# Kernel optimization log

Measured on AMD Instinct MI355X. Metric: run time of the kernel, lower is better.

The kernel has to match this reference:

```python
import jax, jax.numpy as jnp
import numpy as np

NUM_SEQS = 128
TOTAL_TOKENS = 65536
HIDDEN = 768
FF = 3072
EPS = 1e-12  # torch F.normalize default eps


def _make_prompt_lens(rng: np.random.Generator) -> np.ndarray:
    # Ragged lengths in [64, 960], adjusted so they sum exactly to TOTAL_TOKENS.
    lens = rng.integers(64, 960, size=NUM_SEQS).astype(np.int64)
    lens = np.maximum(1, (lens * (TOTAL_TOKENS / lens.sum())).astype(np.int64))
    lens[-1] += TOTAL_TOKENS - lens.sum()
    assert lens.sum() == TOTAL_TOKENS and (lens > 0).all()
    return lens


def setup_inputs() -> dict:
    key = jax.random.key(0)
    k1, k2, k3 = jax.random.split(key, 3)
    hidden_states = jax.random.normal(k1, (TOTAL_TOKENS, HIDDEN), dtype=jnp.float32)
    prompt_lens = jnp.asarray(_make_prompt_lens(np.random.default_rng(0)))
    W1 = jax.random.normal(k2, (FF, HIDDEN), dtype=jnp.float32) * (HIDDEN ** -0.5)
    W2 = jax.random.normal(k3, (HIDDEN, FF), dtype=jnp.float32) * (FF ** -0.5)
    return {"hidden_states": hidden_states, "prompt_lens": prompt_lens, "W1": W1, "W2": W2}


def reference(hidden_states, prompt_lens, W1, W2):
    # hidden_states: [T, H]; prompt_lens: [S] summing to T.
    T = hidden_states.shape[0]
    S = prompt_lens.shape[0]
    # segment id of each token: index of first cumsum strictly greater than position
    seg_ids = jnp.searchsorted(jnp.cumsum(prompt_lens), jnp.arange(T), side="right")
    sums = jax.ops.segment_sum(hidden_states, seg_ids, num_segments=S)  # [S, H]
    pooled = sums / prompt_lens[:, None].astype(hidden_states.dtype)     # mean pool
    h = jnp.einsum("sh,fh->sf", pooled, W1)   # dense1: 768 -> 3072 (no bias)
    h = jnp.einsum("sf,hf->sh", h, W2)        # dense2: 3072 -> 768 (no bias)
    norm = jnp.linalg.norm(h, ord=2, axis=-1, keepdims=True)
    return h / jnp.maximum(norm, EPS)         # L2 normalize, [S, H]
```

## Files before the change

### kernel.cpp

```cpp
#include <hip/hip_runtime.h>

#define TOK   65536
#define HID   768
#define NSEQ  128
#define FFD   3072
#define PCH   32
#define NPCH  (TOK / PCH)
#define KS1   8
#define KCH1  96
#define KS2   32
#define KCH2  96

__device__ __forceinline__ void add4(float4& a, const float4 b) {
  a.x += b.x; a.y += b.y; a.z += b.z; a.w += b.w;
}

__device__ __forceinline__ void scan_lens(const int* __restrict__ lens, int* sc, int tid) {
  if (tid < NSEQ) sc[tid] = lens[tid];
  __syncthreads();
  for (int off = 1; off < NSEQ; off <<= 1) {
    int v = 0;
    if (tid < NSEQ && tid >= off) v = sc[tid - off];
    __syncthreads();
    if (tid < NSEQ) sc[tid] += v;
    __syncthreads();
  }
}

__global__ __launch_bounds__(192, 6) void pool_part(
    const float* __restrict__ x, const int* __restrict__ lens,
    float* __restrict__ plo, float* __restrict__ phi) {
  __shared__ int sc[NSEQ];
  const int tid = threadIdx.x;
  scan_lens(lens, sc, tid);
  const int t0 = blockIdx.x * PCH;
  int lo = 0, hi = NSEQ - 1;
  while (lo < hi) { int mid = (lo + hi) >> 1; if (sc[mid] <= t0) lo = mid + 1; else hi = mid; }
  const int segend = sc[lo];
  const float4* p = (const float4*)x + (size_t)t0 * (HID / 4) + tid;
  float4* dlo = (float4*)plo + (size_t)blockIdx.x * (HID / 4) + tid;

  if (segend >= t0 + PCH) {
    float4 a0 = make_float4(0.f,0.f,0.f,0.f), a1 = a0, a2 = a0, a3 = a0;
    #pragma unroll
    for (int i = 0; i < PCH; i += 4) {
      add4(a0, p[(size_t)(i+0) * (HID/4)]);
      add4(a1, p[(size_t)(i+1) * (HID/4)]);
      add4(a2, p[(size_t)(i+2) * (HID/4)]);
      add4(a3, p[(size_t)(i+3) * (HID/4)]);
    }
    add4(a0, a1); add4(a2, a3); add4(a0, a2);
    *dlo = a0;
  } else {
    const int n0 = segend - t0;
    float4 a0 = make_float4(0.f,0.f,0.f,0.f), a1 = a0;
    for (int i = 0;  i < n0;  ++i) add4(a0, p[(size_t)i * (HID/4)]);
    for (int i = n0; i < PCH; ++i) add4(a1, p[(size_t)i * (HID/4)]);
    *dlo = a0;
    *((float4*)phi + (size_t)blockIdx.x * (HID/4) + tid) = a1;
  }
}

__global__ __launch_bounds__(192) void pool_reduce(
    const int* __restrict__ lens, const float* __restrict__ plo,
    const float* __restrict__ phi, float* __restrict__ pooled) {
  __shared__ int sc[NSEQ];
  const int tid = threadIdx.x;
  scan_lens(lens, sc, tid);
  const int s = blockIdx.x;
  const int st = s ? sc[s - 1] : 0;
  const int en = sc[s];
  const int c0 = st >> 5, c1 = (en - 1) >> 5;
  const float4* lo4 = (const float4*)plo;
  const float4* hi4 = (const float4*)phi;
  float4 acc = make_float4(0.f,0.f,0.f,0.f);
  for (int c = c0; c <= c1; ++c) {
    const float4* src = (c == c0 && (st & (PCH - 1))) ? hi4 : lo4;
    add4(acc, src[(size_t)c * (HID / 4) + tid]);
  }
  const float inv = 1.0f / (float)(en - st);
  float4 r;
  r.x = acc.x * inv; r.y = acc.y * inv; r.z = acc.z * inv; r.w = acc.w * inv;
  ((float4*)pooled)[(size_t)s * (HID / 4) + tid] = r;
}

__global__ __launch_bounds__(256) void gemm_nt(
    const float* __restrict__ A, const float* __restrict__ B,
    float* __restrict__ Cp, int N, int Kt, int kch) {
  __shared__ float As[16][132];
  __shared__ float Bs[16][36];

  const int tid = threadIdx.x;
  const int f0 = blockIdx.x * 32;
  const int k0 = blockIdx.y * kch;
  float* C = Cp + (size_t)blockIdx.y * NSEQ * N;
  const int fx = (tid & 7) * 4;
  const int sy = (tid >> 3) * 4;
  const int sA = tid >> 2;
  const int kA = (tid & 3) * 4;
  const int fB = tid >> 2;

  const float* pA0 = A + (size_t)sA * Kt + k0 + kA;
  const float* pA1 = pA0 + (size_t)64 * Kt;
  const float* pB  = B + (size_t)(f0 + fB) * Kt + k0 + kA;

  float4 va0 = *(const float4*)pA0;
  float4 va1 = *(const float4*)pA1;
  float4 vb = make_float4(0.f,0.f,0.f,0.f);
  if (tid < 128) vb = *(const float4*)pB;

  float acc[4][4];
  #pragma unroll
  for (int i = 0; i < 4; ++i)
    #pragma unroll
    for (int j = 0; j < 4; ++j) acc[i][j] = 0.f;

  const int nch = kch >> 4;
  for (int c = 0; c < nch; ++c) {
    As[kA + 0][sA]      = va0.x; As[kA + 1][sA]      = va0.y;
    As[kA + 2][sA]      = va0.z; As[kA + 3][sA]      = va0.w;
    As[kA + 0][sA + 64] = va1.x; As[kA + 1][sA + 64] = va1.y;
    As[kA + 2][sA + 64] = va1.z; As[kA + 3][sA + 64] = va1.w;
    if (tid < 128) {
      Bs[kA + 0][fB] = vb.x; Bs[kA + 1][fB] = vb.y;
      Bs[kA + 2][fB] = vb.z; Bs[kA + 3][fB] = vb.w;
    }
    __syncthreads();
    if (c + 1 < nch) {
      va0 = *(const float4*)(pA0 + (c + 1) * 16);
      va1 = *(const float4*)(pA1 + (c + 1) * 16);
      if (tid < 128) vb = *(const float4*)(pB + (c + 1) * 16);
    }
    #pragma unroll
    for (int kk = 0; kk < 16; ++kk) {
      const float4 aa = *(const float4*)&As[kk][sy];
      const float4 bb = *(const float4*)&Bs[kk][fx];
      acc[0][0] += aa.x*bb.x; acc[0][1] += aa.x*bb.y; acc[0][2] += aa.x*bb.z; acc[0][3] += aa.x*bb.w;
      acc[1][0] += aa.y*bb.x; acc[1][1] += aa.y*bb.y; acc[1][2] += aa.y*bb.z; acc[1][3] += aa.y*bb.w;
      acc[2][0] += aa.z*bb.x; acc[2][1] += aa.z*bb.y; acc[2][2] += aa.z*bb.z; acc[2][3] += aa.z*bb.w;
      acc[3][0] += aa.w*bb.x; acc[3][1] += aa.w*bb.y; acc[3][2] += aa.w*bb.z; acc[3][3] += aa.w*bb.w;
    }
    __syncthreads();
  }
  #pragma unroll
  for (int i = 0; i < 4; ++i)
    *(float4*)(C + (size_t)(sy + i) * N + f0 + fx) =
        make_float4(acc[i][0], acc[i][1], acc[i][2], acc[i][3]);
}

__global__ __launch_bounds__(256) void reduce_h1(
    const float* __restrict__ h1p, float* __restrict__ h1) {
  const size_t i = (size_t)blockIdx.x * 256 + threadIdx.x;
  const float4* src = (const float4*)h1p;
  float4 a = src[i];
  #pragma unroll
  for (int p = 1; p < KS1; ++p) add4(a, src[i + (size_t)p * (NSEQ * FFD / 4)]);
  ((float4*)h1)[i] = a;
}

__global__ __launch_bounds__(256) void norm_kernel(
    const float* __restrict__ outp, float* __restrict__ out) {
  const int s = blockIdx.x;
  const int tid = threadIdx.x;
  float v[3];
  #pragma unroll
  for (int j = 0; j < 3; ++j) {
    const int c = tid + 256 * j;
    float a = 0.f;
    #pragma unroll
    for (int p = 0; p < KS2; ++p) a += outp[((size_t)p * NSEQ + s) * HID + c];
    v[j] = a;
  }
  float ss = v[0]*v[0] + v[1]*v[1] + v[2]*v[2];
  #pragma unroll
  for (int off = 32; off > 0; off >>= 1) ss += __shfl_down(ss, off, 64);
  __shared__ float wsum[4];
  if ((tid & 63) == 0) wsum[tid >> 6] = ss;
  __syncthreads();
  const float tot = wsum[0] + wsum[1] + wsum[2] + wsum[3];
  const float scale = 1.0f / fmaxf(sqrtf(tot), 1e-12f);
  #pragma unroll
  for (int j = 0; j < 3; ++j) out[(size_t)s * HID + tid + 256 * j] = v[j] * scale;
}

extern "C" void kernel_launch(void* const* d_in, const int* in_sizes, int n_in,
                              void* d_out, int out_size, void* d_ws, size_t ws_size,
                              hipStream_t stream) {
  const float* x    = (const float*)d_in[0];
  const int*   lens = (const int*)d_in[1];
  const float* W1   = (const float*)d_in[2];
  const float* W2   = (const float*)d_in[3];
  float* out = (float*)d_out;

  float* plo    = (float*)d_ws;
  float* phi    = plo + (size_t)NPCH * HID;
  float* pooled = phi + (size_t)NPCH * HID;
  float* h1p    = pooled + (size_t)NSEQ * HID;
  float* h1     = h1p + (size_t)KS1 * NSEQ * FFD;
  float* outp   = h1 + (size_t)NSEQ * FFD;

  pool_part<<<NPCH, 192, 0, stream>>>(x, lens, plo, phi);
  pool_reduce<<<NSEQ, 192, 0, stream>>>(lens, plo, phi, pooled);
  gemm_nt<<<dim3(FFD / 32, KS1), 256, 0, stream>>>(pooled, W1, h1p, FFD, HID, KCH1);
  reduce_h1<<<NSEQ * FFD / 4 / 256, 256, 0, stream>>>(h1p, h1);
  gemm_nt<<<dim3(HID / 32, KS2), 256, 0, stream>>>(h1, W2, outp, HID, FFD, KCH2);
  norm_kernel<<<NSEQ, 256, 0, stream>>>(outp, out);
}
```

Measured before the change: 345.7 us.

## Replace split-K partial buffers and reduction kernel with atomic accumulation

```diff
diff --git a/kernel.cpp b/kernel.cpp
--- a/kernel.cpp
+++ b/kernel.cpp
@@ -10,6 +10,7 @@
 #define KCH1  96
 #define KS2   32
 #define KCH2  96
+#define ZF4   (NSEQ * (FFD + HID) / 4)
 
 __device__ __forceinline__ void add4(float4& a, const float4 b) {
   a.x += b.x; a.y += b.y; a.z += b.z; a.w += b.w;
@@ -29,9 +30,12 @@
 
 __global__ __launch_bounds__(192, 6) void pool_part(
     const float* __restrict__ x, const int* __restrict__ lens,
-    float* __restrict__ plo, float* __restrict__ phi) {
+    float* __restrict__ plo, float* __restrict__ phi,
+    float* __restrict__ zbuf) {
   __shared__ int sc[NSEQ];
   const int tid = threadIdx.x;
+  const size_t gtid = (size_t)blockIdx.x * 192 + tid;
+  if (gtid < ZF4) ((float4*)zbuf)[gtid] = make_float4(0.f, 0.f, 0.f, 0.f);
   scan_lens(lens, sc, tid);
   const int t0 = blockIdx.x * PCH;
   int lo = 0, hi = NSEQ - 1;
@@ -86,14 +90,13 @@
 
 __global__ __launch_bounds__(256) void gemm_nt(
     const float* __restrict__ A, const float* __restrict__ B,
-    float* __restrict__ Cp, int N, int Kt, int kch) {
+    float* __restrict__ C, int N, int Kt, int kch) {
   __shared__ float As[16][132];
   __shared__ float Bs[16][36];
 
   const int tid = threadIdx.x;
   const int f0 = blockIdx.x * 32;
   const int k0 = blockIdx.y * kch;
-  float* C = Cp + (size_t)blockIdx.y * NSEQ * N;
   const int fx = (tid & 7) * 4;
   const int sy = (tid >> 3) * 4;
   const int sA = tid >> 2;
@@ -143,34 +146,22 @@
     __syncthreads();
   }
   #pragma unroll
-  for (int i = 0; i < 4; ++i)
-    *(float4*)(C + (size_t)(sy + i) * N + f0 + fx) =
-        make_float4(acc[i][0], acc[i][1], acc[i][2], acc[i][3]);
-}
-
-__global__ __launch_bounds__(256) void reduce_h1(
-    const float* __restrict__ h1p, float* __restrict__ h1) {
-  const size_t i = (size_t)blockIdx.x * 256 + threadIdx.x;
-  const float4* src = (const float4*)h1p;
-  float4 a = src[i];
-  #pragma unroll
-  for (int p = 1; p < KS1; ++p) add4(a, src[i + (size_t)p * (NSEQ * FFD / 4)]);
-  ((float4*)h1)[i] = a;
+  for (int i = 0; i < 4; ++i) {
+    float* dst = C + (size_t)(sy + i) * N + f0 + fx;
+    atomicAdd(dst + 0, acc[i][0]);
+    atomicAdd(dst + 1, acc[i][1]);
+    atomicAdd(dst + 2, acc[i][2]);
+    atomicAdd(dst + 3, acc[i][3]);
+  }
 }
 
 __global__ __launch_bounds__(256) void norm_kernel(
-    const float* __restrict__ outp, float* __restrict__ out) {
+    const float* __restrict__ h, float* __restrict__ out) {
   const int s = blockIdx.x;
   const int tid = threadIdx.x;
   float v[3];
   #pragma unroll
-  for (int j = 0; j < 3; ++j) {
-    const int c = tid + 256 * j;
-    float a = 0.f;
-    #pragma unroll
-    for (int p = 0; p < KS2; ++p) a += outp[((size_t)p * NSEQ + s) * HID + c];
-    v[j] = a;
-  }
+  for (int j = 0; j < 3; ++j) v[j] = h[(size_t)s * HID + tid + 256 * j];
   float ss = v[0]*v[0] + v[1]*v[1] + v[2]*v[2];
   #pragma unroll
   for (int off = 32; off > 0; off >>= 1) ss += __shfl_down(ss, off, 64);
@@ -195,14 +186,12 @@
   float* plo    = (float*)d_ws;
   float* phi    = plo + (size_t)NPCH * HID;
   float* pooled = phi + (size_t)NPCH * HID;
-  float* h1p    = pooled + (size_t)NSEQ * HID;
-  float* h1     = h1p + (size_t)KS1 * NSEQ * FFD;
-  float* outp   = h1 + (size_t)NSEQ * FFD;
+  float* h1     = pooled + (size_t)NSEQ * HID;
+  float* outacc = h1 + (size_t)NSEQ * FFD;
 
-  pool_part<<<NPCH, 192, 0, stream>>>(x, lens, plo, phi);
+  pool_part<<<NPCH, 192, 0, stream>>>(x, lens, plo, phi, h1);
   pool_reduce<<<NSEQ, 192, 0, stream>>>(lens, plo, phi, pooled);
-  gemm_nt<<<dim3(FFD / 32, KS1), 256, 0, stream>>>(pooled, W1, h1p, FFD, HID, KCH1);
-  reduce_h1<<<NSEQ * FFD / 4 / 256, 256, 0, stream>>>(h1p, h1);
-  gemm_nt<<<dim3(HID / 32, KS2), 256, 0, stream>>>(h1, W2, outp, HID, FFD, KCH2);
-  norm_kernel<<<NSEQ, 256, 0, stream>>>(outp, out);
+  gemm_nt<<<dim3(FFD / 32, KS1), 256, 0, stream>>>(pooled, W1, h1, FFD, HID, KCH1);
+  gemm_nt<<<dim3(HID / 32, KS2), 256, 0, stream>>>(h1, W2, outacc, HID, FFD, KCH2);
+  norm_kernel<<<NSEQ, 256, 0, stream>>>(outacc, out);
 }
```

Result: slower. 404.5 us (+17.0%).
